# Kernel tuning notes

Hardware: AMD Instinct MI355X
Metric: run time of the kernel (lower is better)

## Reference

```python
import jax, jax.numpy as jnp
import numpy as np

PS = 3        # patch_size
RATE = 2      # rate
FS = 3        # fuse_kernel_size
SS = 10.0     # softmax_scale
PAD = (PS - 1) // 2       # tl.calc_padding(ps, 1)
FUSE_PAD = (FS - 1) // 2  # tl.calc_padding(fs, 1)
EPS = 1e-4


def extract_patches(x, ps, stride, pad):
    """x: (B,C,H,W) -> (B, L, C, ps, ps); L row-major over output positions (== F.unfold order)."""
    B, C, H, W = x.shape
    xp = jnp.pad(x, ((0, 0), (0, 0), (pad, pad), (pad, pad)))
    oh = (H + 2 * pad - ps) // stride + 1
    ow = (W + 2 * pad - ps) // stride + 1
    rows = []
    for dy in range(ps):  # small fixed loop (ps=3)
        cols = []
        for dx in range(ps):
            cols.append(xp[:, :, dy:dy + (oh - 1) * stride + 1:stride,
                              dx:dx + (ow - 1) * stride + 1:stride])
        rows.append(jnp.stack(cols, axis=2))           # (B,C,ps,oh,ow)
    p = jnp.stack(rows, axis=2)                        # (B,C,ps,ps,oh,ow)
    return p.reshape(B, C, ps, ps, oh * ow).transpose(0, 4, 1, 2, 3)


def diag_fuse(S, fs, pad):
    """conv2d of (N,N) 'image' with identity fs x fs kernel (diagonal smoothing)."""
    N = S.shape[0]
    Sp = jnp.pad(S, ((pad, pad), (pad, pad)))
    out = Sp[0:N, 0:N]
    for k in range(1, fs):  # fs=3, tiny fixed loop
        out = out + Sp[k:k + N, k:k + N]
    return out


def fuse_scores(S, hr, wr):
    L = hr * wr
    S = diag_fuse(S, FS, FUSE_PAD)
    S = S.reshape(hr, wr, hr, wr).transpose(1, 0, 3, 2).reshape(L, L)
    S = diag_fuse(S, FS, FUSE_PAD)
    S = S.reshape(wr, hr, wr, hr).transpose(1, 0, 3, 2).reshape(L, L)
    return S


def contextual_attention(f_o, b_o, mask_o):
    B, c, h, w = f_o.shape
    # nearest downsample by 1/rate == strided slice
    f = f_o[:, :, ::RATE, ::RATE]
    b = b_o[:, :, ::RATE, ::RATE]
    m = mask_o[:, :, ::RATE, ::RATE]
    hr, wr = f.shape[2], f.shape[3]
    L = hr * wr

    fg = extract_patches(f, PS, 1, PAD)        # (B,L,c,ps,ps) foreground neighborhoods
    bs = extract_patches(b, PS, 1, PAD)        # (B,L,c,ps,ps) shrunk bg patches
    bi = extract_patches(b_o, PS, RATE, PAD)   # (B,L,c,ps,ps) full-res bg patches

    bnorm = jnp.maximum(jnp.sqrt(jnp.sum(bs * bs, axis=(2, 3, 4))), EPS)  # (B,L)
    bsn = bs / bnorm[:, :, None, None, None]

    # score[b,p,q] = <normalized bg patch p, fg neighborhood at position q>
    S = jnp.einsum('bpcij,bqcij->bpq', bsn, fg)  # (B,L,L)
    S = jax.vmap(lambda s: fuse_scores(s, hr, wr))(S)

    # valid-patch indicator from downsampled mask
    mp = extract_patches(m, PS, 1, PAD)                                   # (B,L,1,ps,ps)
    valid = (jnp.mean(mp, axis=(2, 3, 4)) == 0.0).astype(f_o.dtype)       # (B,L)

    score = S.reshape(B, L, hr, wr) * valid[:, :, None, None]
    score = jax.nn.softmax(score * SS, axis=1) * valid[:, :, None, None]

    # conv_transpose2d(score, bi, stride=RATE, padding=PAD, output_padding=1) / 4
    wgt = jnp.flip(bi.transpose(0, 2, 1, 3, 4), axis=(-2, -1))  # (B,c,L,ps,ps)
    pad_cfg = [(PS - 1 - PAD, PS - 1 - PAD + 1)] * 2            # output_padding on high side

    def agg(s, wk):  # s:(L,hr,wr), wk:(c,L,ps,ps)
        return jax.lax.conv_general_dilated(
            s[None], wk, (1, 1), pad_cfg, lhs_dilation=(RATE, RATE),
            dimension_numbers=('NCHW', 'OIHW', 'NCHW'))[0]

    out = jax.vmap(agg)(score, wgt) / 4.0   # (B,c,h,w)
    return out


def setup_inputs() -> dict:
    key = jax.random.key(0)
    k1, k2, k3 = jax.random.split(key, 3)
    f_o = jax.random.normal(k1, (16, 128, 64, 64), dtype=jnp.float32)
    b_o = jax.random.normal(k2, (16, 128, 64, 64), dtype=jnp.float32)
    mask_o = jax.random.randint(k3, (16, 1, 64, 64), 0, 2).astype(jnp.float32)
    return {"f_o": f_o, "b_o": b_o, "mask_o": mask_o}


def reference(f_o, b_o, mask_o):
    return contextual_attention(f_o, b_o, mask_o)
```

## Files before the change

kernel.cpp:

```cpp
#include <hip/hip_runtime.h>
#include <cmath>

#define CC 128
#define HH 64
#define WWI 64
#define LL 1024
#define NB 16
#define MM 1152
#define KC 384
#define TPD 1156

#define SLAB      2977808ul
#define OFF_TP    0
#define OFF_S3T   0
#define OFF_W     0
#define OFF_S2    1336336
#define OFF_SCORET 1336336
#define OFF_POOL  2384912
#define OFF_N2    2974736
#define OFF_BNORM 2975760
#define OFF_VALID 2976784

#define NHROW 132
#define NH1 (NHROW * TPD)
#define NHALO (NH1 + 1024 * NHROW)

typedef __bf16 bf16x8 __attribute__((ext_vector_type(8)));
typedef __bf16 bf16x4 __attribute__((ext_vector_type(4)));
typedef float f32x4 __attribute__((ext_vector_type(4)));

#define GLDS(g, l) __builtin_amdgcn_global_load_lds( \
    (const __attribute__((address_space(1))) unsigned int*)(const void*)(g), \
    (__attribute__((address_space(3))) unsigned int*)(void*)(l), 16, 0, 0)

__global__ __launch_bounds__(256) void k_prep(const float* __restrict__ f_o,
                                              const float* __restrict__ b_o,
                                              float* __restrict__ ws,
                                              int b0, int aff) {
    int bz, uy;
    if (aff) { int g = blockIdx.x; bz = g & 15; uy = g >> 4; }
    else     { bz = blockIdx.y; uy = blockIdx.x; }
    int gb = b0 + bz;
    __shared__ float lf[128 * 33];
    __shared__ float lb[128 * 33];
    __shared__ float red[8 * 32];
    int tid = threadIdx.x;
    int ux = tid & 31, co = tid >> 5;
    size_t pix = (size_t)(2 * uy) * WWI + 2 * ux;
    const float* fbp = f_o + (size_t)gb * CC * HH * WWI + pix;
    const float* bbp = b_o + (size_t)gb * CC * HH * WWI + pix;
#pragma unroll
    for (int pass = 0; pass < 16; pass++) {
        int c = pass * 8 + co;
        lf[c * 33 + ux] = fbp[(size_t)c * HH * WWI];
        lb[c * 33 + ux] = bbp[(size_t)c * HH * WWI];
    }
    __syncthreads();
    int ux2 = tid >> 3, cg = (tid & 7) * 16;
    int u = uy * 32 + ux2;
    __bf16* bcat = (__bf16*)(ws + (size_t)bz * SLAB + OFF_POOL) + (size_t)u * KC;
    __bf16* fcat = bcat + 393216;
    float s2 = 0.f;
#pragma unroll
    for (int k = 0; k < 16; k++) {
        int c = cg + k;
        float fv = lf[c * 33 + ux2];
        float bv = lb[c * 33 + ux2];
        __bf16 fhi = (__bf16)fv; __bf16 flo = (__bf16)(fv - (float)fhi);
        __bf16 bhi = (__bf16)bv; __bf16 blo = (__bf16)(bv - (float)bhi);
        bcat[c] = bhi; bcat[128 + c] = bhi; bcat[256 + c] = blo;
        fcat[c] = fhi; fcat[128 + c] = flo; fcat[256 + c] = fhi;
        s2 += bv * bv;
    }
    red[(tid & 7) * 32 + ux2] = s2;
    __syncthreads();
    if (tid < 32) {
        float s = 0.f;
#pragma unroll
        for (int k = 0; k < 8; k++) s += red[k * 32 + tid];
        ws[(size_t)bz * SLAB + OFF_N2 + uy * 32 + tid] = s;
    }
}

__global__ __launch_bounds__(256) void k_bnorm_valid(float* __restrict__ ws,
                                                     const float* __restrict__ mask,
                                                     int b0, int aff) {
    int g = blockIdx.x;
    int bz, pc;
    if (aff) { bz = g & 15; pc = g >> 4; }
    else     { bz = g >> 2; pc = g & 3; }
    int p = pc * 256 + threadIdx.x;
    int gb = b0 + bz;
    int py = p >> 5, px = p & 31;
    const float* mb = mask + (size_t)gb * HH * WWI;
    const float* n2 = ws + (size_t)bz * SLAB + OFF_N2;
    float s = 0.f, msum = 0.f;
#pragma unroll
    for (int dy = -1; dy <= 1; dy++) {
#pragma unroll
        for (int dx = -1; dx <= 1; dx++) {
            int py2 = py + dy, px2 = px + dx;
            if ((unsigned)py2 < 32u && (unsigned)px2 < 32u) {
                s    += n2[(py2 << 5) | px2];
                msum += mb[(2 * py2) * WWI + 2 * px2];
            }
        }
    }
    ws[(size_t)bz * SLAB + OFF_BNORM + p] = fmaxf(sqrtf(s), 1e-4f);
    ws[(size_t)bz * SLAB + OFF_VALID + p] = (msum == 0.0f) ? 1.0f : 0.0f;
}

__device__ __forceinline__ int halo_idx(int k) {
    if (k < 34) return k;
    if (k < 68) return 1122 + (k - 34);
    if (k < 100) return 34 * (k - 100 + 33);
    return 34 * (k - 132 + 33) + 33;
}

template<int KTOT>
__device__ __forceinline__ void gemm_core(const __bf16* __restrict__ Ab,
                                          const __bf16* __restrict__ Bb,
                                          int lda, int ldb, int m0, int n0,
                                          __bf16* As, __bf16* Bs,
                                          f32x4 acc[4][4]) {
    int t = threadIdx.x;
    int lane = t & 63, w = t >> 6;
    int rsub = lane >> 3;
    int g8   = ((lane & 7) ^ (rsub & 7)) * 8;
    int lm = lane & 15, kgf = lane >> 4;
    int wm = (w & 1) * 64, wn = (w >> 1) * 64;

#define ISSUE(kt, buf) do {                                                   \
    int k0_ = (kt) * 64;                                                      \
    _Pragma("unroll")                                                         \
    for (int ci = 0; ci < 4; ci++) {                                          \
        int rb = ci * 32 + w * 8;                                             \
        int r  = rb + rsub;                                                   \
        GLDS(Ab + (size_t)(m0 + r) * lda + k0_ + g8, &As[(buf) + rb * 64]);   \
        GLDS(Bb + (size_t)(n0 + r) * ldb + k0_ + g8, &Bs[(buf) + rb * 64]);   \
    } } while (0)

#define COMPUTE(curoff) do {                                                  \
    _Pragma("unroll")                                                         \
    for (int s2 = 0; s2 < 2; s2++) {                                          \
        bf16x8 af[4], bfr[4];                                                 \
        _Pragma("unroll")                                                     \
        for (int i = 0; i < 4; i++)                                           \
            af[i] = *(const bf16x8*)&As[(curoff) + (wm + i * 16 + lm) * 64 +  \
                                        (((s2 * 4 + kgf) ^ (lm & 7)) * 8)];   \
        _Pragma("unroll")                                                     \
        for (int j = 0; j < 4; j++)                                           \
            bfr[j] = *(const bf16x8*)&Bs[(curoff) + (wn + j * 16 + lm) * 64 + \
                                         (((s2 * 4 + kgf) ^ (lm & 7)) * 8)];  \
        _Pragma("unroll")                                                     \
        for (int i = 0; i < 4; i++)                                           \
            _Pragma("unroll")                                                 \
            for (int j = 0; j < 4; j++)                                       \
                acc[i][j] = __builtin_amdgcn_mfma_f32_16x16x32_bf16(          \
                    af[i], bfr[j], acc[i][j], 0, 0, 0);                       \
    } } while (0)

    const int NIT = KTOT / 64;

    ISSUE(0, 0);
    ISSUE(1, 8192);

#pragma unroll 2
    for (int it = 0; it < NIT - 2; it++) {
        int cur = (it & 1) * 8192;
        asm volatile("s_waitcnt vmcnt(8)" ::: "memory");
        __builtin_amdgcn_sched_barrier(0);
        __builtin_amdgcn_s_barrier();
        COMPUTE(cur);
        __builtin_amdgcn_s_barrier();
        ISSUE(it + 2, cur);
    }
    asm volatile("s_waitcnt vmcnt(8)" ::: "memory");
    __builtin_amdgcn_sched_barrier(0);
    __builtin_amdgcn_s_barrier();
    COMPUTE(((NIT - 2) & 1) * 8192);
    __builtin_amdgcn_s_barrier();
    asm volatile("s_waitcnt vmcnt(0)" ::: "memory");
    __builtin_amdgcn_sched_barrier(0);
    __builtin_amdgcn_s_barrier();
    COMPUTE(((NIT - 1) & 1) * 8192);

#undef ISSUE
#undef COMPUTE
}

__global__ __launch_bounds__(256) void k_gemm_T_mfma(float* __restrict__ ws, int swz) {
    int bz, m0, n0;
    if (swz) {
        bz = blockIdx.x + 8 * (blockIdx.z & 1);
        m0 = blockIdx.y * 128;
        n0 = (blockIdx.z >> 1) * 128;
    } else {
        bz = blockIdx.z; m0 = blockIdx.y * 128; n0 = blockIdx.x * 128;
    }
    const __bf16* Ab = (const __bf16*)(ws + (size_t)bz * SLAB + OFF_POOL);
    const __bf16* Bb = Ab + 393216;
    float* Tp = ws + (size_t)bz * SLAB + OFF_TP;
    __shared__ __align__(16) __bf16 As[2 * 128 * 64];
    __shared__ __align__(16) __bf16 Bs[2 * 128 * 64];
    f32x4 acc[4][4];
#pragma unroll
    for (int i = 0; i < 4; i++)
#pragma unroll
        for (int j = 0; j < 4; j++) acc[i][j] = (f32x4)0.0f;
    gemm_core<KC>(Ab, Bb, KC, KC, m0, n0, As, Bs, acc);
    int lane = threadIdx.x & 63, w = threadIdx.x >> 6;
    int lm = lane & 15, kgf = lane >> 4;
    int wm = (w & 1) * 64, wn = (w >> 1) * 64;
#pragma unroll
    for (int i = 0; i < 4; i++) {
#pragma unroll
        for (int r = 0; r < 4; r++) {
            int m = m0 + wm + i * 16 + kgf * 4 + r;
            float* dst = Tp + (size_t)(((m >> 5) + 1) * 34 + (m & 31) + 1) * TPD;
#pragma unroll
            for (int j = 0; j < 4; j++) {
                int v = n0 + wn + j * 16 + lm;
                dst[((v >> 5) + 1) * 34 + (v & 31) + 1] = acc[i][j][r];
            }
        }
    }
    int cb = (m0 >> 7) * 8 + (n0 >> 7);
    for (int h = cb * 256 + (int)threadIdx.x; h < NHALO; h += 64 * 256) {
        if (h < NH1) {
            int R = halo_idx(h / TPD);
            Tp[(size_t)R * TPD + (h % TPD)] = 0.f;
        } else {
            int t2 = h - NH1;
            int ir = t2 / NHROW;
            int R  = 34 * (1 + (ir >> 5)) + 1 + (ir & 31);
            int C  = halo_idx(t2 % NHROW);
            Tp[(size_t)R * TPD + C] = 0.f;
        }
    }
}

__global__ __launch_bounds__(512, 2) void k_gemm_W192(float* __restrict__ ws) {
    int d = blockIdx.x;
    int logical = (d & 7) * 48 + (d >> 3);
    int bz  = logical / 24;
    int t24 = logical % 24;
    int m0 = (t24 >> 2) * 192;
    int n0 = (t24 & 3) * 256;
    const __bf16* Ab = (const __bf16*)(ws + (size_t)bz * SLAB + OFF_POOL);
    const __bf16* Bb = (const __bf16*)(ws + (size_t)bz * SLAB + OFF_SCORET);
    __bf16* Wb = (__bf16*)(ws + (size_t)bz * SLAB + OFF_W);
    __shared__ __align__(16) __bf16 As[2 * 192 * 64];
    __shared__ __align__(16) __bf16 Bs[2 * 256 * 64];

    int t = threadIdx.x;
    int lane = t & 63, w = t >> 6;
    int rsub = lane >> 3;
    int g8   = ((lane & 7) ^ (rsub & 7)) * 8;
    int lm = lane & 15, kgf = lane >> 4;
    int wr = (w >> 2) * 96;
    int wc = (w & 3) * 64;

    f32x4 acc[6][4];
#pragma unroll
    for (int i = 0; i < 6; i++)
#pragma unroll
        for (int j = 0; j < 4; j++) acc[i][j] = (f32x4)0.0f;

#define WSTAGE(nbA, nbB, k1_) do {                                            \
    _Pragma("unroll")                                                         \
    for (int ci = 0; ci < 3; ci++) {                                          \
        int rb = ci * 64 + w * 8;                                             \
        GLDS(Ab + (size_t)(m0 + rb + rsub) * LL + (k1_) + g8,                 \
             &As[(nbA) + rb * 64]);                                           \
    }                                                                         \
    _Pragma("unroll")                                                         \
    for (int ci = 0; ci < 4; ci++) {                                          \
        int rb = ci * 64 + w * 8;                                             \
        GLDS(Bb + (size_t)(n0 + rb + rsub) * LL + (k1_) + g8,                 \
             &Bs[(nbB) + rb * 64]);                                           \
    } } while (0)

#define RD_A(mh, boA) do {                                                    \
    _Pragma("unroll")                                                         \
    for (int mi = 0; mi < 3; mi++)                                            \
        _Pragma("unroll")                                                     \
        for (int ks = 0; ks < 2; ks++)                                        \
            af[mi][ks] = *(const bf16x8*)&As[(boA) +                          \
                (wr + (mh) * 48 + mi * 16 + lm) * 64 +                        \
                (((ks * 4 + kgf) ^ (lm & 7)) * 8)];                           \
    } while (0)

#define RD_B(njlo, boB) do {                                                  \
    _Pragma("unroll")                                                         \
    for (int nj = 0; nj < 2; nj++)                                            \
        _Pragma("unroll")                                                     \
        for (int ks = 0; ks < 2; ks++)                                        \
            bfr[(njlo) + nj][ks] = *(const bf16x8*)&Bs[(boB) +                \
                (wc + ((njlo) + nj) * 16 + lm) * 64 +                         \
                (((ks * 4 + kgf) ^ (lm & 7)) * 8)];                           \
    } while (0)

#define QMFMA(mb, njlo) do {                                                  \
    __builtin_amdgcn_s_setprio(1);                                            \
    _Pragma("unroll")                                                         \
    for (int ks = 0; ks < 2; ks++)                                            \
        _Pragma("unroll")                                                     \
        for (int mi = 0; mi < 3; mi++)                                        \
            _Pragma("unroll")                                                 \
            for (int nj = 0; nj < 2; nj++)                                    \
                acc[(mb) + mi][(njlo) + nj] =                                 \
                    __builtin_amdgcn_mfma_f32_16x16x32_bf16(                  \
                        af[mi][ks], bfr[(njlo) + nj][ks],                     \
                        acc[(mb) + mi][(njlo) + nj], 0, 0, 0);                \
    __builtin_amdgcn_s_setprio(0);                                            \
    } while (0)

    WSTAGE(0, 0, 0);
    asm volatile("s_waitcnt vmcnt(0)" ::: "memory");
    __builtin_amdgcn_sched_barrier(0);
    __builtin_amdgcn_s_barrier();

#pragma unroll 2
    for (int kt = 0; kt < 16; kt++) {
        int boA = (kt & 1) * 12288, boB = (kt & 1) * 16384;
        int nbA = boA ^ 12288, nbB = boB ^ 16384;
        bf16x8 af[3][2], bfr[4][2];
        if (kt < 15) WSTAGE(nbA, nbB, (kt + 1) * 64);
        RD_A(0, boA);
        RD_B(0, boB);
        QMFMA(0, 0);
        RD_B(2, boB);
        QMFMA(0, 2);
        RD_A(1, boA);
        QMFMA(3, 2);
        QMFMA(3, 0);
        if (kt < 15) {
            asm volatile("s_waitcnt vmcnt(0)" ::: "memory");
            __builtin_amdgcn_sched_barrier(0);
            __builtin_amdgcn_s_barrier();
        }
    }

#undef WSTAGE
#undef RD_A
#undef RD_B
#undef QMFMA

#pragma unroll
    for (int mf = 0; mf < 6; mf++) {
#pragma unroll
        for (int r = 0; r < 4; r++) {
            int m = m0 + wr + mf * 16 + kgf * 4 + r;
            __bf16* dst = Wb + (size_t)m * LL + n0 + wc + lm;
#pragma unroll
            for (int nj = 0; nj < 4; nj++)
                dst[nj * 16] = (__bf16)acc[mf][nj][r];
        }
    }
}

__global__ __launch_bounds__(256) void k_gemm_W_mfma(float* __restrict__ ws, int swz) {
    int bz, m0, n0;
    if (swz) {
        bz = blockIdx.x + 8 * (blockIdx.z & 1);
        m0 = blockIdx.y * 128;
        n0 = (blockIdx.z >> 1) * 128;
    } else {
        bz = blockIdx.z; m0 = blockIdx.y * 128; n0 = blockIdx.x * 128;
    }
    const __bf16* Ab = (const __bf16*)(ws + (size_t)bz * SLAB + OFF_POOL);
    const __bf16* Bb = (const __bf16*)(ws + (size_t)bz * SLAB + OFF_SCORET);
    __bf16* Wb = (__bf16*)(ws + (size_t)bz * SLAB + OFF_W);
    __shared__ __align__(16) __bf16 As[2 * 128 * 64];
    __shared__ __align__(16) __bf16 Bs[2 * 128 * 64];
    f32x4 acc[4][4];
#pragma unroll
    for (int i = 0; i < 4; i++)
#pragma unroll
        for (int j = 0; j < 4; j++) acc[i][j] = (f32x4)0.0f;
    gemm_core<LL>(Ab, Bb, LL, LL, m0, n0, As, Bs, acc);
    int lane = threadIdx.x & 63, w = threadIdx.x >> 6;
    int lm = lane & 15, kgf = lane >> 4;
    int wm = (w & 1) * 64, wn = (w >> 1) * 64;
#pragma unroll
    for (int i = 0; i < 4; i++) {
#pragma unroll
        for (int r = 0; r < 4; r++) {
            int m = m0 + wm + i * 16 + kgf * 4 + r;
            __bf16* dst = Wb + (size_t)m * LL + n0 + wn + lm;
#pragma unroll
            for (int j = 0; j < 4; j++)
                dst[j * 16] = (__bf16)acc[i][j][r];
        }
    }
}

__global__ __launch_bounds__(256) void k_s12(float* __restrict__ ws, int aff) {
    int bz, i0;
    if (aff) { int g = blockIdx.x; bz = g & 15; i0 = (g >> 4) * 8; }
    else     { bz = blockIdx.y; i0 = blockIdx.x * 8; }
    const float* Tp = ws + (size_t)bz * SLAB + OFF_TP;
    const float* bn = ws + (size_t)bz * SLAB + OFF_BNORM;
    float* S2 = ws + (size_t)bz * SLAB + OFF_S2;
    __shared__ float Dsh[10][1024];
    int tid = threadIdx.x;
    for (int rl = 0; rl < 10; rl++) {
        int r = i0 - 1 + rl;
        if ((unsigned)r >= 1024u) continue;
        float invr = 1.0f / bn[r];
        size_t rbase = (size_t)(((r >> 5) + 1) * 34 + (r & 31) + 1) * TPD;
#pragma unroll
        for (int so = 0; so < 4; so++) {
            int s = so * 256 + tid;
            const float* cb = Tp + rbase + ((s >> 5) + 1) * 34 + (s & 31) + 1;
            float d = 0.f;
#pragma unroll
            for (int dy = -1; dy <= 1; dy++)
#pragma unroll
                for (int dx = -1; dx <= 1; dx++)
                    d += cb[dy * (34 * TPD + 34) + dx * (TPD + 1)];
            Dsh[rl][s] = d * invr;
        }
    }
    __syncthreads();
#pragma unroll
    for (int il = 0; il < 8; il++) {
        int i = i0 + il;
        float* orow = S2 + (size_t)i * LL;
#pragma unroll
        for (int jo = 0; jo < 4; jo++) {
            int j = jo * 256 + tid;
            float acc = 0.f;
#pragma unroll
            for (int k1 = -1; k1 <= 1; k1++) {
                int r = i + k1, s = j + k1;
                if ((unsigned)r < 1024u && (unsigned)s < 1024u)
                    acc += Dsh[il + 1 + k1][s];
            }
            orow[j] = acc;
        }
    }
}

__global__ __launch_bounds__(256) void k_st3t(float* __restrict__ ws, int aff) {
    int bz, p0, q0;
    if (aff) {
        int g = blockIdx.x; bz = g & 15;
        int tile = g >> 4; p0 = (tile >> 4) * 64; q0 = (tile & 15) * 64;
    } else {
        bz = blockIdx.z; p0 = blockIdx.y * 64; q0 = blockIdx.x * 64;
    }
    const float* ib = ws + (size_t)bz * SLAB + OFF_S2;
    float* ob = ws + (size_t)bz * SLAB + OFF_S3T;
    __shared__ float tile[64][65];
    int t = threadIdx.x;
#pragma unroll
    for (int it = 0; it < 16; it++) {
        int e = it * 256 + t;
        int pl = e >> 6, ql = e & 63;
        int p = p0 + pl, q = q0 + ql;
        int sp = ((p & 31) << 5) | (p >> 5);
        int sq = ((q & 31) << 5) | (q >> 5);
        float acc = 0.f;
#pragma unroll
        for (int k = -1; k <= 1; k++) {
            int tp = sp + k, tq = sq + k;
            if ((unsigned)tp < 1024u && (unsigned)tq < 1024u) {
                int row = ((tp & 31) << 5) | (tp >> 5);
                int col = ((tq & 31) << 5) | (tq >> 5);
                acc += ib[(size_t)row * LL + col];
            }
        }
        tile[pl][ql] = acc;
    }
    __syncthreads();
#pragma unroll
    for (int it = 0; it < 16; it++) {
        int e = it * 256 + t;
        int ql = e >> 6, pl = e & 63;
        ob[(size_t)(q0 + ql) * LL + p0 + pl] = tile[pl][ql];
    }
}

__global__ __launch_bounds__(256) void k_softmax_bf(float* __restrict__ ws, int aff) {
    int bz, q;
    if (aff) {
        int g = blockIdx.x; bz = g & 15;
        q = (g >> 4) * 4 + (threadIdx.x >> 6);
    } else {
        bz = blockIdx.z;
        q = blockIdx.x * 4 + (threadIdx.x >> 6);
    }
    int lane = threadIdx.x & 63;
    const float* row = ws + (size_t)bz * SLAB + OFF_S3T + (size_t)q * LL;
    const float* vb  = ws + (size_t)bz * SLAB + OFF_VALID;
    __bf16* orow = (__bf16*)(ws + (size_t)bz * SLAB + OFF_SCORET) + (size_t)q * LL;

    float4 v[4], vl[4];
#pragma unroll
    for (int i = 0; i < 4; i++) {
        int p = lane * 4 + i * 256;
        float4 s = *(const float4*)(row + p);
        float4 m = *(const float4*)(vb + p);
        v[i] = {s.x * m.x, s.y * m.y, s.z * m.z, s.w * m.w};
        vl[i] = m;
    }
    float mx = -1e30f;
#pragma unroll
    for (int i = 0; i < 4; i++)
        mx = fmaxf(mx, fmaxf(fmaxf(v[i].x, v[i].y), fmaxf(v[i].z, v[i].w)));
#pragma unroll
    for (int k = 1; k < 64; k <<= 1)
        mx = fmaxf(mx, __shfl_xor(mx, k, 64));
    float sum = 0.f;
    float4 e[4];
#pragma unroll
    for (int i = 0; i < 4; i++) {
        e[i].x = __expf(10.f * (v[i].x - mx));
        e[i].y = __expf(10.f * (v[i].y - mx));
        e[i].z = __expf(10.f * (v[i].z - mx));
        e[i].w = __expf(10.f * (v[i].w - mx));
        sum += e[i].x + e[i].y + e[i].z + e[i].w;
    }
#pragma unroll
    for (int k = 1; k < 64; k <<= 1)
        sum += __shfl_xor(sum, k, 64);
    float inv = 1.0f / sum;
#pragma unroll
    for (int i = 0; i < 4; i++) {
        bf16x4 o;
        o[0] = (__bf16)(e[i].x * inv * vl[i].x);
        o[1] = (__bf16)(e[i].y * inv * vl[i].y);
        o[2] = (__bf16)(e[i].z * inv * vl[i].z);
        o[3] = (__bf16)(e[i].w * inv * vl[i].w);
        *(bf16x4*)(orow + lane * 4 + i * 256) = o;
    }
}

__global__ __launch_bounds__(256) void k_makeA(const float* __restrict__ b_o,
                                               float* __restrict__ ws,
                                               int b0, int aff) {
    int c, bz;
    if (aff) { int g = blockIdx.x; bz = g & 15; c = g >> 4; }
    else     { c = blockIdx.x; bz = blockIdx.y; }
    int gb = b0 + bz;
    __shared__ float img[64][65];
    int t = threadIdx.x;
    const float4* src = (const float4*)(b_o + (size_t)(gb * CC + c) * HH * WWI);
#pragma unroll
    for (int it = 0; it < 4; it++) {
        int idx = it * 256 + t;
        float4 v = src[idx];
        int row = idx >> 4, col4 = (idx & 15) * 4;
        img[row][col4] = v.x; img[row][col4 + 1] = v.y;
        img[row][col4 + 2] = v.z; img[row][col4 + 3] = v.w;
    }
    __syncthreads();
    __bf16* Ab = (__bf16*)(ws + (size_t)bz * SLAB + OFF_POOL) + (size_t)c * 9 * LL;
    int py = t >> 3, px4 = (t & 7) * 4;
#pragma unroll
    for (int jy = 0; jy < 3; jy++) {
        int row = 2 * py + jy - 1;
        bool rok = (unsigned)row < 64u;
#pragma unroll
        for (int jx = 0; jx < 3; jx++) {
            bf16x4 o;
#pragma unroll
            for (int e = 0; e < 4; e++) {
                int col = 2 * (px4 + e) + jx - 1;
                float v = (rok && (unsigned)col < 64u) ? img[rok ? row : 0][(unsigned)col < 64u ? col : 0] : 0.f;
                o[e] = (__bf16)v;
            }
            *(bf16x4*)(Ab + (size_t)(jy * 3 + jx) * LL + t * 4) = o;
        }
    }
}

__global__ __launch_bounds__(256) void k_gather(const float* __restrict__ ws,
                                                float* __restrict__ outp,
                                                int b0, int aff) {
    int t;
    if (aff) {
        int g = blockIdx.x;
        int bz_ = g & 15;
        t = (bz_ << 19) + (g >> 4) * 256 + threadIdx.x;
    } else {
        t = blockIdx.x * 256 + threadIdx.x;
    }
    int ox = t & 63, oy = (t >> 6) & 63, c = (t >> 12) & 127, bz = t >> 19;
    const __bf16* Wb = (const __bf16*)(ws + (size_t)bz * SLAB + OFF_W);
    int qyA = (oy + 1) >> 1;
    int jyA = (oy & 1) ? 0 : 1;
    int vA  = (qyA < 32);
    int qyB = (oy - 1) >> 1;
    int vB  = (oy & 1);
    int qxA = (ox + 1) >> 1;
    int jxA = (ox & 1) ? 0 : 1;
    int uA  = (qxA < 32);
    int qxB = (ox - 1) >> 1;
    int uB  = (ox & 1);
    const __bf16* base = Wb + (size_t)c * 9 * LL;
    float s = 0.f;
    if (vA && uA) s += (float)base[(size_t)(jyA * 3 + jxA) * LL + qyA * 32 + qxA];
    if (vA && uB) s += (float)base[(size_t)(jyA * 3 + 2)   * LL + qyA * 32 + qxB];
    if (vB && uA) s += (float)base[(size_t)(2 * 3 + jxA)   * LL + qyB * 32 + qxA];
    if (vB && uB) s += (float)base[(size_t)(2 * 3 + 2)     * LL + qyB * 32 + qxB];
    outp[((size_t)((b0 + bz) * CC + c) * HH + oy) * WWI + ox] = 0.25f * s;
}

extern "C" void kernel_launch(void* const* d_in, const int* in_sizes, int n_in,
                              void* d_out, int out_size, void* d_ws, size_t ws_size,
                              hipStream_t stream) {
    (void)in_sizes; (void)n_in; (void)out_size;
    const float* f_o  = (const float*)d_in[0];
    const float* b_o  = (const float*)d_in[1];
    const float* mask = (const float*)d_in[2];
    float* out = (float*)d_out;

    int G = (int)(ws_size / (SLAB * sizeof(float)));
    if (G < 1) G = 1;
    if (G > NB) G = NB;
    float* ws = (float*)d_ws;

    for (int b0 = 0; b0 < NB; b0 += G) {
        int Gc = NB - b0 < G ? NB - b0 : G;
        if (Gc == NB) {
            k_prep<<<dim3(512), 256, 0, stream>>>(f_o, b_o, ws, 0, 1);
            k_bnorm_valid<<<dim3(64), 256, 0, stream>>>(ws, mask, 0, 1);
            k_gemm_T_mfma<<<dim3(8, 8, 16), 256, 0, stream>>>(ws, 1);
            k_s12<<<dim3(2048), 256, 0, stream>>>(ws, 1);
            k_st3t<<<dim3(4096), 256, 0, stream>>>(ws, 1);
            k_softmax_bf<<<dim3(4096), 256, 0, stream>>>(ws, 1);
            k_makeA<<<dim3(2048), 256, 0, stream>>>(b_o, ws, 0, 1);
            k_gemm_W192<<<dim3(384), 512, 0, stream>>>(ws);
            k_gather<<<dim3(32768), 256, 0, stream>>>(ws, out, 0, 1);
        } else {
            k_prep<<<dim3(32, Gc), 256, 0, stream>>>(f_o, b_o, ws, b0, 0);
            k_bnorm_valid<<<dim3(Gc * 4), 256, 0, stream>>>(ws, mask, b0, 0);
            k_gemm_T_mfma<<<dim3(8, 8, Gc), 256, 0, stream>>>(ws, 0);
            k_s12<<<dim3(128, Gc), 256, 0, stream>>>(ws, 0);
            k_st3t<<<dim3(16, 16, Gc), 256, 0, stream>>>(ws, 0);
            k_softmax_bf<<<dim3(256, 1, Gc), 256, 0, stream>>>(ws, 0);
            k_makeA<<<dim3(CC, Gc), 256, 0, stream>>>(b_o, ws, b0, 0);
            k_gemm_W_mfma<<<dim3(8, 9, Gc), 256, 0, stream>>>(ws, 0);
            k_gather<<<dim3(Gc * 2048), 256, 0, stream>>>(ws, out, b0, 0);
        }
    }
}
```

Measured before the change: 349.1 us.

## Store intermediate score rows in transposed spatial order to simplify second fuse pass

Writes the first diagonal-fuse output rows, the valid mask and the pooled background patches in a spatially transposed (x-major) index order. The second fuse pass in k_st3t can then read contiguous rows directly instead of permuting both row and column indices. This is meant to improve memory coalescing in the second fuse pass. It relies on every consumer (softmax, gather) agreeing on the new ordering.

```diff
diff --git a/kernel.cpp b/kernel.cpp
--- a/kernel.cpp
+++ b/kernel.cpp
@@ -25,6 +25,8 @@
 #define NH1 (NHROW * TPD)
 #define NHALO (NH1 + 1024 * NHROW)
 
+#define BS(x) ((((x) & 31) << 5) | ((x) >> 5))
+
 typedef __bf16 bf16x8 __attribute__((ext_vector_type(8)));
 typedef __bf16 bf16x4 __attribute__((ext_vector_type(4)));
 typedef float f32x4 __attribute__((ext_vector_type(4)));
@@ -32,6 +34,7 @@
 #define GLDS(g, l) __builtin_amdgcn_global_load_lds( \
     (const __attribute__((address_space(1))) unsigned int*)(const void*)(g), \
     (__attribute__((address_space(3))) unsigned int*)(void*)(l), 16, 0, 0)
+
 
 __global__ __launch_bounds__(256) void k_prep(const float* __restrict__ f_o,
                                               const float* __restrict__ b_o,
@@ -107,7 +110,7 @@
         }
     }
     ws[(size_t)bz * SLAB + OFF_BNORM + p] = fmaxf(sqrtf(s), 1e-4f);
-    ws[(size_t)bz * SLAB + OFF_VALID + p] = (msum == 0.0f) ? 1.0f : 0.0f;
+    ws[(size_t)bz * SLAB + OFF_VALID + BS(p)] = (msum == 0.0f) ? 1.0f : 0.0f;
 }
 
 __device__ __forceinline__ int halo_idx(int k) {
@@ -427,7 +430,7 @@
 #pragma unroll
     for (int il = 0; il < 8; il++) {
         int i = i0 + il;
-        float* orow = S2 + (size_t)i * LL;
+        float* orow = S2 + (size_t)BS(i) * LL;
 #pragma unroll
         for (int jo = 0; jo < 4; jo++) {
             int j = jo * 256 + tid;
@@ -444,12 +447,12 @@
 }
 
 __global__ __launch_bounds__(256) void k_st3t(float* __restrict__ ws, int aff) {
-    int bz, p0, q0;
+    int bz, b0, q0;
     if (aff) {
         int g = blockIdx.x; bz = g & 15;
-        int tile = g >> 4; p0 = (tile >> 4) * 64; q0 = (tile & 15) * 64;
+        int tile_ = g >> 4; b0 = (tile_ >> 4) * 64; q0 = (tile_ & 15) * 64;
     } else {
-        bz = blockIdx.z; p0 = blockIdx.y * 64; q0 = blockIdx.x * 64;
+        bz = blockIdx.z; b0 = blockIdx.y * 64; q0 = blockIdx.x * 64;
     }
     const float* ib = ws + (size_t)bz * SLAB + OFF_S2;
     float* ob = ws + (size_t)bz * SLAB + OFF_S3T;
@@ -458,28 +461,24 @@
 #pragma unroll
     for (int it = 0; it < 16; it++) {
         int e = it * 256 + t;
-        int pl = e >> 6, ql = e & 63;
-        int p = p0 + pl, q = q0 + ql;
-        int sp = ((p & 31) << 5) | (p >> 5);
-        int sq = ((q & 31) << 5) | (q >> 5);
+        int bl = e >> 6, ql = e & 63;
+        int b = b0 + bl, q = q0 + ql;
+        int sq = BS(q);
         float acc = 0.f;
 #pragma unroll
         for (int k = -1; k <= 1; k++) {
-            int tp = sp + k, tq = sq + k;
-            if ((unsigned)tp < 1024u && (unsigned)tq < 1024u) {
-                int row = ((tp & 31) << 5) | (tp >> 5);
-                int col = ((tq & 31) << 5) | (tq >> 5);
-                acc += ib[(size_t)row * LL + col];
-            }
-        }
-        tile[pl][ql] = acc;
+            int tp = b + k, tq = sq + k;
+            if ((unsigned)tp < 1024u && (unsigned)tq < 1024u)
+                acc += ib[(size_t)tp * LL + BS(tq)];
+        }
+        tile[bl][ql] = acc;
     }
     __syncthreads();
 #pragma unroll
     for (int it = 0; it < 16; it++) {
         int e = it * 256 + t;
-        int ql = e >> 6, pl = e & 63;
-        ob[(size_t)(q0 + ql) * LL + p0 + pl] = tile[pl][ql];
+        int ql = e >> 6, bl = e & 63;
+        ob[(size_t)(q0 + ql) * LL + b0 + bl] = tile[bl][ql];
     }
 }
 
@@ -558,18 +557,19 @@
     }
     __syncthreads();
     __bf16* Ab = (__bf16*)(ws + (size_t)bz * SLAB + OFF_POOL) + (size_t)c * 9 * LL;
-    int py = t >> 3, px4 = (t & 7) * 4;
+    int px = t >> 3, py4 = (t & 7) * 4;
 #pragma unroll
     for (int jy = 0; jy < 3; jy++) {
-        int row = 2 * py + jy - 1;
-        bool rok = (unsigned)row < 64u;
 #pragma unroll
         for (int jx = 0; jx < 3; jx++) {
+            int col = 2 * px + jx - 1;
+            bool cok = (unsigned)col < 64u;
             bf16x4 o;
 #pragma unroll
             for (int e = 0; e < 4; e++) {
-                int col = 2 * (px4 + e) + jx - 1;
-                float v = (rok && (unsigned)col < 64u) ? img[rok ? row : 0][(unsigned)col < 64u ? col : 0] : 0.f;
+                int row = 2 * (py4 + e) + jy - 1;
+                float v = (cok && (unsigned)row < 64u)
+                            ? img[(unsigned)row < 64u ? row : 0][cok ? col : 0] : 0.f;
                 o[e] = (__bf16)v;
             }
             *(bf16x4*)(Ab + (size_t)(jy * 3 + jx) * LL + t * 4) = o;
```

Result: no change. 346.6 us (-0.7%).
